# Performance work log

Hardware: AMD Instinct MI355X
Metric: run time of the kernel (lower is better)

Reference implementation:

```python
import jax, jax.numpy as jnp
import numpy as np

Z, DIM_IN, DIM_TS, DIM_OUT = 4096, 256, 2048, 256


def setup_inputs() -> dict:
    key = jax.random.key(0)
    k1, k2, k3 = jax.random.split(key, 3)
    features = jax.random.normal(k1, (Z, DIM_IN), dtype=jnp.float32)
    # Dense stand-in for the sparse CG buffer T: [dim_ts, dim_in * dim_in]
    T = jax.random.normal(k2, (DIM_TS, DIM_IN * DIM_IN), dtype=jnp.float32) * 0.02
    # KernelLinear output (learned mixing weights): [dim_out, dim_ts]
    W = jax.random.normal(k3, (DIM_OUT, DIM_TS), dtype=jnp.float32) * 0.02
    return {"features": features, "T": T, "W": W}


def reference(features, T, W):
    # features: [..., dim_in]; flatten leading dims as in the torch module
    *size, n = features.shape
    x = features.reshape(-1, n)                       # [z, i]
    # (T.t() @ W.T).T == W @ T ; reshape to [k, i, j]
    K = (W @ T).reshape(W.shape[0], n, n)             # [k, i, j]
    # per-sample bilinear (quadratic) form
    out = jnp.einsum('kij,zi,zj->zk', K, x, x)        # [z, k]
    return out.reshape(*size, -1)
```

## Files before the change

kernel.cpp:

```cpp
#include <hip/hip_runtime.h>

#define ZDIM 4096
#define DIN  256
#define DTS  2048
#define DOUT 256
#define CDIM 65536
#define SPLIT 16
#define NJS  8
#define NI   16
#define NST  (NJS * NI)
#define ZP   256
#define TILE_B 8192
#define CH_B  ((size_t)NST * 2 * TILE_B)

typedef float fv4 __attribute__((ext_vector_type(4)));
typedef __bf16 bv8 __attribute__((ext_vector_type(8)));
typedef unsigned short u16;
typedef u16 uv8 __attribute__((ext_vector_type(8)));
typedef u16 uv4 __attribute__((ext_vector_type(4)));

union BC  { __bf16 b; u16 u; };
union VC8 { uv8 u; bv8 b; };
union FU  { unsigned u; float f; };

static __device__ __forceinline__ u16  f2b(float f){ BC c; c.b=(__bf16)f; return c.u; }
static __device__ __forceinline__ float bu(u16 v){ FU c; c.u = ((unsigned)v) << 16; return c.f; }
static __device__ __forceinline__ bv8  asb(uv8 x){ VC8 c; c.u=x; return c.b; }
static __device__ __forceinline__ uv8  pack8(fv4 a, fv4 b){
  uv8 p;
  p[0]=f2b(a[0]); p[1]=f2b(a[1]); p[2]=f2b(a[2]); p[3]=f2b(a[3]);
  p[4]=f2b(b[0]); p[5]=f2b(b[1]); p[6]=f2b(b[2]); p[7]=f2b(b[3]);
  return p;
}


__global__ __launch_bounds__(512, 2) void k_wt(const float* __restrict__ W,
                                               const float* __restrict__ T,
                                               u16* __restrict__ Km) {
  __shared__ u16 Al[256 * 40];
  __shared__ u16 Bl[32 * 128];
  const int tid  = threadIdx.x;
  const int lane = tid & 63;
  const int wave = tid >> 6;
  const int wk = (wave >> 1) * 64;
  const int wc = (wave & 1) * 64;
  const int cb = blockIdx.x * 128;
  const int ar = lane & 15, tg = lane >> 4;

  fv4 acc[4][4];
#pragma unroll
  for (int m = 0; m < 4; ++m)
#pragma unroll
    for (int n = 0; n < 4; ++n)
#pragma unroll
      for (int r = 0; r < 4; ++r) acc[m][n][r] = 0.f;

  for (int t0 = 0; t0 < DTS; t0 += 32) {
#pragma unroll
    for (int p = 0; p < 2; ++p) {
      int oct = tid + p * 512;
      int kr = oct >> 2, ts = (oct & 3) * 8;
      const float* src = W + (size_t)kr * DTS + t0 + ts;
      fv4 a = *(const fv4*)src, b = *(const fv4*)(src + 4);
      *(uv8*)&Al[kr * 40 + ts] = pack8(a, b);
    }
    {
      int tr = tid >> 4, co = (tid & 15) * 8;
      const float* src = T + (size_t)(t0 + tr) * CDIM + cb + co;
      fv4 a = *(const fv4*)src, b = *(const fv4*)(src + 4);
      *(uv8*)&Bl[tr * 128 + co] = pack8(a, b);
    }
    __syncthreads();
    bv8 af[4];
#pragma unroll
    for (int m = 0; m < 4; ++m)
      af[m] = asb(*(const uv8*)&Al[(wk + m * 16 + ar) * 40 + tg * 8]);
#pragma unroll
    for (int n = 0; n < 4; ++n) {
      uv8 bu2;
#pragma unroll
      for (int e = 0; e < 8; ++e)
        bu2[e] = Bl[(tg * 8 + e) * 128 + wc + n * 16 + ar];
      bv8 bf = asb(bu2);
#pragma unroll
      for (int m = 0; m < 4; ++m)
        acc[m][n] = __builtin_amdgcn_mfma_f32_16x16x32_bf16(af[m], bf, acc[m][n], 0, 0, 0);
    }
    __syncthreads();
  }
  const int ig = cb >> 8;
  const int j0 = cb & 255;
#pragma unroll
  for (int m = 0; m < 4; ++m)
#pragma unroll
    for (int n = 0; n < 4; ++n) {
      int j  = j0 + wc + n * 16;
      int js = j >> 5;
      int jj = j & 31;
      int sc = ig >> 4, il = ig & 15;
#pragma unroll
      for (int r = 0; r < 4; ++r) {
        int kr = wk + m * 16 + tg * 4 + r;
        int kh = kr >> 7, kp = kr & 127;
        size_t tb = (size_t)sc * CH_B +
                    (size_t)((js * 16 + il) * 2 + kh) * TILE_B;
        int e = kp * 64 + (jj + ar) * 2;
        e ^= ((e >> 7) & 7) << 4;
        *(u16*)((char*)Km + tb + e) = f2b(acc[m][n][r]);
      }
    }
}

__global__ __launch_bounds__(512, 2) void k_bil(const float* __restrict__ X,
                                                const u16* __restrict__ Km,
                                                u16* __restrict__ P) {
  __shared__ u16 Kl[4 * 4096];
  __shared__ float Xt[16 * 256];
  const int tid  = threadIdx.x;
  const int lane = tid & 63;
  const int wave = tid >> 6;
  const int wz   = (wave >> 1) * 64;
  const int wkp  = (wave & 1) * 64;
  const int bid  = blockIdx.x;
  const int s    = bid & 15;
  const int kh   = (bid >> 4) & 1;
  const int z0   = (bid >> 5) * ZP;
  const int i0   = s * NI;
  const int ar   = lane & 15, tg = lane >> 4;

  const char* chunk = (const char*)Km + (size_t)s * CH_B;
#define TOFF(t) ((size_t)(((t) * 2) + kh) * TILE_B)

  for (int idx = tid; idx < 16 * 256; idx += 512) {
    int ii = idx >> 8, z = idx & 255;
    Xt[idx] = X[(size_t)(z0 + z) * DIN + i0 + ii];
  }
#pragma unroll
  for (int t = 0; t < 3; ++t)
    __builtin_amdgcn_global_load_lds(
        (const __attribute__((address_space(1))) void*)(chunk + TOFF(t) + (size_t)tid * 16),
        (__attribute__((address_space(3))) void*)((char*)Kl + t * TILE_B + tid * 16), 16, 0, 0);
  __syncthreads();

  int boff[4], xoff[4];
#pragma unroll
  for (int n = 0; n < 4; ++n) {
    int kpp = wkp + n * 16 + ar;
    int e = kpp * 64 + tg * 16;
    boff[n] = e ^ (((e >> 7) & 7) << 4);
  }
#pragma unroll
  for (int m = 0; m < 4; ++m) xoff[m] = wz + m * 16 + ar;

  fv4 acc[4][4];
#pragma unroll
  for (int m = 0; m < 4; ++m)
#pragma unroll
    for (int n = 0; n < 4; ++n)
#pragma unroll
      for (int r = 0; r < 4; ++r) acc[m][n][r] = 0.f;

  int ca = 0, cd = 3;

#define KB_ITER(ST, II, ISSUE, BARW)                                            \
  {                                                                             \
    if (ISSUE)                                                                  \
      __builtin_amdgcn_global_load_lds(                                         \
          (const __attribute__((address_space(1))) void*)(chunk +               \
              TOFF((ST) + 3) + (size_t)tid * 16),                               \
          (__attribute__((address_space(3))) void*)((char*)Kl +                 \
              cd * TILE_B + tid * 16), 16, 0, 0);                               \
    uv8 ap_[4];                                                                 \
    _Pragma("unroll")                                                           \
    for (int m_ = 0; m_ < 4; ++m_) {                                            \
      float xi_ = Xt[(II) * 256 + xoff[m_]];                                    \
      _Pragma("unroll")                                                         \
      for (int e_ = 0; e_ < 8; ++e_) ap_[m_][e_] = f2b(xi_ * bu(af[m_][e_]));   \
    }                                                                           \
    _Pragma("unroll")                                                           \
    for (int n_ = 0; n_ < 4; ++n_) {                                            \
      bv8 bf_ = asb(*(const uv8*)((const char*)Kl + ca * TILE_B + boff[n_]));   \
      _Pragma("unroll")                                                         \
      for (int m_ = 0; m_ < 4; ++m_)                                            \
        acc[m_][n_] = __builtin_amdgcn_mfma_f32_16x16x32_bf16(                  \
            asb(ap_[m_]), bf_, acc[m_][n_], 0, 0, 0);                           \
    }                                                                           \
    if ((BARW) >= 0) {                                                          \
      if ((BARW) == 2)      asm volatile("s_waitcnt vmcnt(2)" ::: "memory");    \
      else if ((BARW) == 1) asm volatile("s_waitcnt vmcnt(1)" ::: "memory");    \
      else                  asm volatile("s_waitcnt vmcnt(0)" ::: "memory");    \
      __builtin_amdgcn_s_barrier();                                             \
      asm volatile("" ::: "memory");                                            \
    }                                                                           \
    ca = (ca + 1) & 3; cd = (cd + 1) & 3;                                       \
  }

  for (int js = 0; js < 7; ++js) {
    uv8 af[4];
#pragma unroll
    for (int m = 0; m < 4; ++m) {
      const float* row = X + (size_t)(z0 + wz + m * 16 + ar) * DIN + js * 32 + tg * 8;
      af[m] = pack8(*(const fv4*)row, *(const fv4*)(row + 4));
    }
#pragma unroll
    for (int i = 0; i < 16; ++i) KB_ITER(js * 16 + i, i, true, 2)
  }
  {
    uv8 af[4];
#pragma unroll
    for (int m = 0; m < 4; ++m) {
      const float* row = X + (size_t)(z0 + wz + m * 16 + ar) * DIN + 7 * 32 + tg * 8;
      af[m] = pack8(*(const fv4*)row, *(const fv4*)(row + 4));
    }
#pragma unroll
    for (int i = 0; i < 13; ++i) KB_ITER(112 + i, i, true, 2)
    KB_ITER(125, 13, false, 1)
    KB_ITER(126, 14, false, 0)
    KB_ITER(127, 15, false, -1)
  }
#undef KB_ITER
#undef TOFF

  u16* dst = P + (size_t)s * (ZDIM * DOUT) + (size_t)z0 * DOUT + kh * 128;
#pragma unroll
  for (int m = 0; m < 4; ++m)
#pragma unroll
    for (int n = 0; n < 4; ++n)
#pragma unroll
      for (int r = 0; r < 4; ++r)
        dst[(size_t)(wz + m * 16 + tg * 4 + r) * DOUT + wkp + n * 16 + ar] =
            f2b(acc[m][n][r]);
}

__global__ __launch_bounds__(256) void k_red(const u16* __restrict__ P,
                                             float* __restrict__ O) {
  size_t idx = ((size_t)blockIdx.x * 256 + threadIdx.x) * 4;
  fv4 acc;
#pragma unroll
  for (int r = 0; r < 4; ++r) acc[r] = 0.f;
#pragma unroll
  for (int p = 0; p < SPLIT; ++p) {
    uv4 v = *(const uv4*)&P[(size_t)p * (ZDIM * DOUT) + idx];
#pragma unroll
    for (int r = 0; r < 4; ++r) acc[r] += bu(v[r]);
  }
  *(fv4*)&O[idx] = acc;
}

extern "C" void kernel_launch(void* const* d_in, const int* in_sizes, int n_in,
                              void* d_out, int out_size, void* d_ws, size_t ws_size,
                              hipStream_t stream) {
  const float* feat = (const float*)d_in[0];
  const float* T    = (const float*)d_in[1];
  const float* W    = (const float*)d_in[2];
  float* out = (float*)d_out;

  u16* Km = (u16*)d_ws;
  u16* P  = (u16*)((char*)d_ws + (size_t)DOUT * CDIM * 2);

  k_wt <<<dim3(512),  dim3(512), 0, stream>>>(W, T, Km);
  k_bil<<<dim3(512),  dim3(512), 0, stream>>>(feat, Km, P);
  k_red<<<dim3(1024), dim3(256), 0, stream>>>(P, out);
}
```

Baseline: 336.4 us.

## Pipeline T tiles via async global-to-LDS loads and pre-convert W to bf16

Adds a prep kernel that converts W to bf16 once, so k_wt reads W fragments straight from global memory instead of staging them through LDS every step. T tiles are streamed into a 4-deep LDS ring with global_load_lds, prefetched three steps ahead, with vmcnt waits and a single barrier per step replacing the two syncthreads. The bf16 conversion of T moves to the LDS read side. This aims to overlap the T stream with MFMA work and remove register round-trips, at the cost of 64 KB of LDS per block, uncached-looking global reads of W, and an extra kernel launch. The Wb scratch reuses the P buffer, which is safe only because k_bil overwrites P after k_wt finishes.

Result: slower. 350.0 us (+4.1%).

```diff
diff --git a/kernel.cpp b/kernel.cpp
--- a/kernel.cpp
+++ b/kernel.cpp
@@ -33,12 +33,18 @@
   return p;
 }
 
-
-__global__ __launch_bounds__(512, 2) void k_wt(const float* __restrict__ W,
+__global__ __launch_bounds__(256) void k_prep(const float* __restrict__ W,
+                                              u16* __restrict__ Wb) {
+  int idx = (blockIdx.x * 256 + threadIdx.x) * 8;
+  fv4 a = *(const fv4*)&W[idx], b = *(const fv4*)&W[idx + 4];
+  *(uv8*)&Wb[idx] = pack8(a, b);
+}
+
+
+__global__ __launch_bounds__(512, 2) void k_wt(const u16* __restrict__ Wb,
                                                const float* __restrict__ T,
                                                u16* __restrict__ Km) {
-  __shared__ u16 Al[256 * 40];
-  __shared__ u16 Bl[32 * 128];
+  __shared__ float Tl[4 * 4096];
   const int tid  = threadIdx.x;
   const int lane = tid & 63;
   const int wave = tid >> 6;
@@ -46,6 +52,24 @@
   const int wc = (wave & 1) * 64;
   const int cb = blockIdx.x * 128;
   const int ar = lane & 15, tg = lane >> 4;
+  const int sr = tid >> 5;
+  const int sc = (tid & 31) * 4;
+
+#define TISSUE(ST, BUF)                                                        \
+  {                                                                            \
+    _Pragma("unroll")                                                          \
+    for (int p_ = 0; p_ < 2; ++p_)                                             \
+      __builtin_amdgcn_global_load_lds(                                        \
+        (const __attribute__((address_space(1))) void*)(                       \
+           T + (size_t)((ST) * 32 + p_ * 16 + sr) * CDIM + cb + sc),           \
+        (__attribute__((address_space(3))) void*)(                             \
+           (char*)Tl + (BUF) * 16384 + p_ * 8192 + tid * 16), 16, 0, 0);       \
+  }
+
+  TISSUE(0, 0) TISSUE(1, 1) TISSUE(2, 2)
+  asm volatile("s_waitcnt vmcnt(4)" ::: "memory");
+  __builtin_amdgcn_s_barrier();
+  asm volatile("" ::: "memory");
 
   fv4 acc[4][4];
 #pragma unroll
@@ -55,39 +79,32 @@
 #pragma unroll
       for (int r = 0; r < 4; ++r) acc[m][n][r] = 0.f;
 
-  for (int t0 = 0; t0 < DTS; t0 += 32) {
-#pragma unroll
-    for (int p = 0; p < 2; ++p) {
-      int oct = tid + p * 512;
-      int kr = oct >> 2, ts = (oct & 3) * 8;
-      const float* src = W + (size_t)kr * DTS + t0 + ts;
-      fv4 a = *(const fv4*)src, b = *(const fv4*)(src + 4);
-      *(uv8*)&Al[kr * 40 + ts] = pack8(a, b);
-    }
-    {
-      int tr = tid >> 4, co = (tid & 15) * 8;
-      const float* src = T + (size_t)(t0 + tr) * CDIM + cb + co;
-      fv4 a = *(const fv4*)src, b = *(const fv4*)(src + 4);
-      *(uv8*)&Bl[tr * 128 + co] = pack8(a, b);
-    }
-    __syncthreads();
+  for (int st = 0; st < 64; ++st) {
+    const int t0 = st * 32;
     bv8 af[4];
 #pragma unroll
     for (int m = 0; m < 4; ++m)
-      af[m] = asb(*(const uv8*)&Al[(wk + m * 16 + ar) * 40 + tg * 8]);
+      af[m] = asb(*(const uv8*)&Wb[(size_t)(wk + m * 16 + ar) * DTS + t0 + tg * 8]);
+    if (st < 61) TISSUE(st + 3, (st + 3) & 3)
+    const float* tl = Tl + (st & 3) * 4096;
 #pragma unroll
     for (int n = 0; n < 4; ++n) {
-      uv8 bu2;
+      uv8 bb;
 #pragma unroll
       for (int e = 0; e < 8; ++e)
-        bu2[e] = Bl[(tg * 8 + e) * 128 + wc + n * 16 + ar];
-      bv8 bf = asb(bu2);
+        bb[e] = f2b(tl[(tg * 8 + e) * 128 + wc + n * 16 + ar]);
+      bv8 bf = asb(bb);
 #pragma unroll
       for (int m = 0; m < 4; ++m)
         acc[m][n] = __builtin_amdgcn_mfma_f32_16x16x32_bf16(af[m], bf, acc[m][n], 0, 0, 0);
     }
-    __syncthreads();
-  }
+    if (st < 61) asm volatile("s_waitcnt vmcnt(2)" ::: "memory");
+    else         asm volatile("s_waitcnt vmcnt(0)" ::: "memory");
+    __builtin_amdgcn_s_barrier();
+    asm volatile("" ::: "memory");
+  }
+#undef TISSUE
+
   const int ig = cb >> 8;
   const int j0 = cb & 255;
 #pragma unroll
@@ -97,12 +114,12 @@
       int j  = j0 + wc + n * 16;
       int js = j >> 5;
       int jj = j & 31;
-      int sc = ig >> 4, il = ig & 15;
+      int sc2 = ig >> 4, il = ig & 15;
 #pragma unroll
       for (int r = 0; r < 4; ++r) {
         int kr = wk + m * 16 + tg * 4 + r;
         int kh = kr >> 7, kp = kr & 127;
-        size_t tb = (size_t)sc * CH_B +
+        size_t tb = (size_t)sc2 * CH_B +
                     (size_t)((js * 16 + il) * 2 + kh) * TILE_B;
         int e = kp * 64 + (jj + ar) * 2;
         e ^= ((e >> 7) & 7) << 4;
@@ -257,8 +274,10 @@
 
   u16* Km = (u16*)d_ws;
   u16* P  = (u16*)((char*)d_ws + (size_t)DOUT * CDIM * 2);
-
-  k_wt <<<dim3(512),  dim3(512), 0, stream>>>(W, T, Km);
-  k_bil<<<dim3(512),  dim3(512), 0, stream>>>(feat, Km, P);
-  k_red<<<dim3(1024), dim3(256), 0, stream>>>(P, out);
-}
+  u16* Wb = P;
+
+  k_prep<<<dim3(256),  dim3(256), 0, stream>>>(W, Wb);
+  k_wt  <<<dim3(512),  dim3(512), 0, stream>>>(Wb, T, Km);
+  k_bil <<<dim3(512),  dim3(512), 0, stream>>>(feat, Km, P);
+  k_red <<<dim3(1024), dim3(256), 0, stream>>>(P, out);
+}
```

## Double-buffer T tiles in k_wt and load W fragments directly from global

Applied to the files above, without the earlier changes.

The W@T GEMM kernel now double-buffers the T tile in shared memory, prefetching the next tile into registers while MFMAs run on the current one. This halves the barriers per step. The W operand is no longer staged through LDS; each wave loads its A fragments straight from global memory and converts them to bf16. The T row stride is padded from 128 to 130 to reduce bank conflicts on the strided column reads. The trade-off is redundant global loads of W across waves and blocks (L2-cached), plus higher register pressure.

Result: slower. 459.6 us (+36.6%).

```diff
diff --git a/kernel.cpp b/kernel.cpp
--- a/kernel.cpp
+++ b/kernel.cpp
@@ -37,8 +37,7 @@
 __global__ __launch_bounds__(512, 2) void k_wt(const float* __restrict__ W,
                                                const float* __restrict__ T,
                                                u16* __restrict__ Km) {
-  __shared__ u16 Al[256 * 40];
-  __shared__ u16 Bl[32 * 128];
+  __shared__ u16 Bl[2][32 * 130];
   const int tid  = threadIdx.x;
   const int lane = tid & 63;
   const int wave = tid >> 6;
@@ -46,6 +45,13 @@
   const int wc = (wave & 1) * 64;
   const int cb = blockIdx.x * 128;
   const int ar = lane & 15, tg = lane >> 4;
+  const int tr = tid >> 4, co = (tid & 15) * 8;
+
+  {
+    const float* src = T + (size_t)tr * CDIM + cb + co;
+    *(uv8*)&Bl[0][tr * 130 + co] = pack8(*(const fv4*)src, *(const fv4*)(src + 4));
+  }
+  __syncthreads();
 
   fv4 acc[4][4];
 #pragma unroll
@@ -55,39 +61,38 @@
 #pragma unroll
       for (int r = 0; r < 4; ++r) acc[m][n][r] = 0.f;
 
-  for (int t0 = 0; t0 < DTS; t0 += 32) {
-#pragma unroll
-    for (int p = 0; p < 2; ++p) {
-      int oct = tid + p * 512;
-      int kr = oct >> 2, ts = (oct & 3) * 8;
-      const float* src = W + (size_t)kr * DTS + t0 + ts;
-      fv4 a = *(const fv4*)src, b = *(const fv4*)(src + 4);
-      *(uv8*)&Al[kr * 40 + ts] = pack8(a, b);
-    }
-    {
-      int tr = tid >> 4, co = (tid & 15) * 8;
-      const float* src = T + (size_t)(t0 + tr) * CDIM + cb + co;
-      fv4 a = *(const fv4*)src, b = *(const fv4*)(src + 4);
-      *(uv8*)&Bl[tr * 128 + co] = pack8(a, b);
-    }
-    __syncthreads();
+  int buf = 0;
+  for (int st = 0; st < 64; ++st) {
+    const int t0 = st * 32;
     bv8 af[4];
 #pragma unroll
-    for (int m = 0; m < 4; ++m)
-      af[m] = asb(*(const uv8*)&Al[(wk + m * 16 + ar) * 40 + tg * 8]);
+    for (int m = 0; m < 4; ++m) {
+      const float* wsrc = W + (size_t)(wk + m * 16 + ar) * DTS + t0 + tg * 8;
+      af[m] = asb(pack8(*(const fv4*)wsrc, *(const fv4*)(wsrc + 4)));
+    }
+    const bool stg = (st < 63);
+    fv4 ta, tb;
+    if (stg) {
+      const float* src = T + (size_t)(t0 + 32 + tr) * CDIM + cb + co;
+      ta = *(const fv4*)src; tb = *(const fv4*)(src + 4);
+    }
 #pragma unroll
     for (int n = 0; n < 4; ++n) {
       uv8 bu2;
 #pragma unroll
       for (int e = 0; e < 8; ++e)
-        bu2[e] = Bl[(tg * 8 + e) * 128 + wc + n * 16 + ar];
+        bu2[e] = Bl[buf][(tg * 8 + e) * 130 + wc + n * 16 + ar];
       bv8 bf = asb(bu2);
 #pragma unroll
       for (int m = 0; m < 4; ++m)
         acc[m][n] = __builtin_amdgcn_mfma_f32_16x16x32_bf16(af[m], bf, acc[m][n], 0, 0, 0);
     }
+    if (stg)
+      *(uv8*)&Bl[buf ^ 1][tr * 130 + co] = pack8(ta, tb);
     __syncthreads();
-  }
+    buf ^= 1;
+  }
+
   const int ig = cb >> 8;
   const int j0 = cb & 255;
 #pragma unroll
@@ -102,11 +107,11 @@
       for (int r = 0; r < 4; ++r) {
         int kr = wk + m * 16 + tg * 4 + r;
         int kh = kr >> 7, kp = kr & 127;
-        size_t tb = (size_t)sc * CH_B +
-                    (size_t)((js * 16 + il) * 2 + kh) * TILE_B;
+        size_t tb2 = (size_t)sc * CH_B +
+                     (size_t)((js * 16 + il) * 2 + kh) * TILE_B;
         int e = kp * 64 + (jj + ar) * 2;
         e ^= ((e >> 7) & 7) << 4;
-        *(u16*)((char*)Km + tb + e) = f2b(acc[m][n][r]);
+        *(u16*)((char*)Km + tb2 + e) = f2b(acc[m][n][r]);
       }
     }
 }
```
